# Kernel tuning notes

Hardware: AMD Instinct MI355X
Metric: run time of the kernel (lower is better)

The kernel has to match this reference:

```python
import jax, jax.numpy as jnp
import numpy as np

NUM_EMBEDDINGS = 8192
EMBEDDING_DIM = 256
COMMITMENT_COST = 0.25


def setup_inputs() -> dict:
    key = jax.random.key(0)
    k1, k2 = jax.random.split(key)
    z_e = jax.random.normal(k1, (16, 2048, EMBEDDING_DIM), dtype=jnp.float32)
    # nn.Embedding init: uniform(-1/K, 1/K)
    codebook = jax.random.uniform(
        k2, (NUM_EMBEDDINGS, EMBEDDING_DIM), dtype=jnp.float32,
        minval=-1.0 / NUM_EMBEDDINGS, maxval=1.0 / NUM_EMBEDDINGS)
    return {"z_e": z_e, "codebook": codebook}


def _nearest_indices(z_flat, codebook):
    # squared euclidean distances; argmin is identical to argmin of cdist
    # z_flat: [T, D], codebook: [K, D] -> dist2: [T, K]
    x2 = jnp.sum(z_flat * z_flat, axis=-1, keepdims=True)          # [T, 1]
    w2 = jnp.sum(codebook * codebook, axis=-1)                      # [K]
    xw = jnp.einsum('td,kd->tk', z_flat, codebook)                  # [T, K]
    dist2 = x2 - 2.0 * xw + w2
    return jnp.argmin(dist2, axis=1)                                # [T]


def reference(z_e, codebook):
    original_shape = z_e.shape
    z_e_flat = z_e.reshape(-1, EMBEDDING_DIM)
    indices = _nearest_indices(z_e_flat, codebook)
    z_q = codebook[indices].reshape(original_shape)
    # straight-through estimator
    z_q_ste = z_e + jax.lax.stop_gradient(z_q - z_e)
    commitment_loss = jnp.mean((z_e - jax.lax.stop_gradient(z_q_ste)) ** 2)
    codebook_loss = jnp.mean((z_q_ste - jax.lax.stop_gradient(z_e)) ** 2)
    loss = codebook_loss + COMMITMENT_COST * commitment_loss
    # codebook usage: fraction of unique indices (jit-friendly via scatter)
    used = jnp.zeros((NUM_EMBEDDINGS,), dtype=jnp.float32).at[indices].set(1.0)
    usage = jnp.sum(used) / NUM_EMBEDDINGS
    return (z_q_ste, loss, usage)
```

## Files before the change

### kernel.cpp

```cpp
#include <hip/hip_runtime.h>
#include <float.h>

#define T_TOTAL 32768
#define KC      8192
#define DIM     256

#define LOSS_IDX  ((size_t)T_TOTAL * DIM)
#define USAGE_IDX (LOSS_IDX + 1)

typedef short s16x8 __attribute__((ext_vector_type(8)));
typedef float f32x4 __attribute__((ext_vector_type(4)));

#define WS_W2    0
#define WS_FLAGS 32768
#define WS_CBF   65536

__device__ __forceinline__ unsigned short f2bf(float f) {
    unsigned int u = __float_as_uint(f);
    u += 0x7FFFu + ((u >> 16) & 1u);
    return (unsigned short)(u >> 16);
}

__global__ __launch_bounds__(256) void vq_prep(const float* __restrict__ cb,
                                               unsigned short* __restrict__ cbb,
                                               float* __restrict__ w2,
                                               int* __restrict__ flags,
                                               float* __restrict__ out) {
    const int blk = blockIdx.x, tid = threadIdx.x;
    size_t i = (size_t)blk * 2048 + (size_t)tid * 8;
    float4 a = *(const float4*)(cb + i);
    float4 b = *(const float4*)(cb + i + 4);
    uint4 o;
    o.x = (unsigned)f2bf(a.x) | ((unsigned)f2bf(a.y) << 16);
    o.y = (unsigned)f2bf(a.z) | ((unsigned)f2bf(a.w) << 16);
    o.z = (unsigned)f2bf(b.x) | ((unsigned)f2bf(b.y) << 16);
    o.w = (unsigned)f2bf(b.z) | ((unsigned)f2bf(b.w) << 16);
    *(uint4*)(cbb + i) = o;
    float s = a.x * a.x + a.y * a.y + a.z * a.z + a.w * a.w
            + b.x * b.x + b.y * b.y + b.z * b.z + b.w * b.w;
    #pragma unroll
    for (int m = 1; m <= 16; m <<= 1) s += __shfl_xor(s, m);
    if ((tid & 31) == 0) w2[blk * 8 + (tid >> 5)] = s;
    if (blk < 32) flags[blk * 256 + tid] = 0;
    if (blk == 0 && tid == 0) { out[LOSS_IDX] = 0.0f; out[USAGE_IDX] = 0.0f; }
}

__global__ __launch_bounds__(512, 2) void vq_main(const unsigned short* __restrict__ cbb,
                                                  const float* __restrict__ w2g,
                                                  const float* __restrict__ z_e,
                                                  const float* __restrict__ cb,
                                                  float* __restrict__ out,
                                                  int* __restrict__ flags) {
    __shared__ unsigned short ca[2][128 * 128];
    __shared__ unsigned long long smin[128];
    __shared__ float wls[8];

    const int tid  = threadIdx.x;
    const int lane = tid & 63;
    const int w    = tid >> 6;
    const int wr   = w >> 2;
    const int wc   = w & 3;
    const int quad = lane >> 4;
    const int l15  = lane & 15;
    const int t0   = blockIdx.x * 128;

    if (tid < 128) smin[tid] = ~0ULL;

    const int srow_off = lane >> 4;
    #define STAGE(CHUNK, KW, P)                                                         \
        {                                                                               \
            _Pragma("unroll")                                                           \
            for (int r = 0; r < 4; ++r) {                                               \
                int rowbase = r * 32 + w * 4;                                           \
                int row = rowbase + srow_off;                                           \
                int src_c = l15 ^ (row & 15);                                           \
                __builtin_amdgcn_global_load_lds(                                       \
                    (const __attribute__((address_space(1))) void*)                     \
                        (cbb + (size_t)((CHUNK) * 128 + row) * DIM + (KW) * 128 + src_c * 8), \
                    (__attribute__((address_space(3))) void*)(ca[P] + rowbase * 128),   \
                    16, 0, 0);                                                          \
            }                                                                           \
        }

    s16x8 af[4][8];
    #pragma unroll
    for (int i = 0; i < 4; ++i) {
        #pragma unroll
        for (int ks = 0; ks < 8; ++ks) {
            const float* p = z_e + (size_t)(t0 + wr * 64 + i * 16 + l15) * DIM + ks * 32 + quad * 8;
            float4 a = *(const float4*)p;
            float4 b = *(const float4*)(p + 4);
            s16x8 v;
            v[0] = (short)f2bf(a.x); v[1] = (short)f2bf(a.y);
            v[2] = (short)f2bf(a.z); v[3] = (short)f2bf(a.w);
            v[4] = (short)f2bf(b.x); v[5] = (short)f2bf(b.y);
            v[6] = (short)f2bf(b.z); v[7] = (short)f2bf(b.w);
            af[i][ks] = v;
        }
    }

    float best[4][4];
    int   bidx[4][4];
    #pragma unroll
    for (int i = 0; i < 4; ++i)
        #pragma unroll
        for (int r = 0; r < 4; ++r) { best[i][r] = FLT_MAX; bidx[i][r] = 0x7FFFFFFF; }

    STAGE(0, 0, 0);

    for (int c = 0; c < 64; ++c) {
        f32x4 acc[4][2];
        #pragma unroll
        for (int i = 0; i < 4; ++i)
            #pragma unroll
            for (int j = 0; j < 2; ++j) acc[i][j] = (f32x4){0.f, 0.f, 0.f, 0.f};

        #pragma unroll
        for (int kw = 0; kw < 2; ++kw) {
            __syncthreads();
            if (kw == 0) {
                STAGE(c, 1, 1);
            } else if (c < 63) {
                STAGE(c + 1, 0, 0);
            }
            #pragma unroll
            for (int kk = 0; kk < 4; ++kk) {
                s16x8 bfr[2];
                #pragma unroll
                for (int j = 0; j < 2; ++j) {
                    int row = wc * 32 + j * 16 + l15;
                    int slot = (kk * 4 + quad) ^ l15;
                    bfr[j] = *(const s16x8*)(ca[kw] + row * 128 + slot * 8);
                }
                #pragma unroll
                for (int i = 0; i < 4; ++i)
                    #pragma unroll
                    for (int j = 0; j < 2; ++j)
                        acc[i][j] = __builtin_amdgcn_mfma_f32_16x16x32_bf16(af[i][kw * 4 + kk], bfr[j], acc[i][j], 0, 0, 0);
            }
        }

        #pragma unroll
        for (int j = 0; j < 2; ++j) {
            int col = c * 128 + wc * 32 + j * 16 + l15;
            float w2v = w2g[col];
            #pragma unroll
            for (int i = 0; i < 4; ++i)
                #pragma unroll
                for (int r = 0; r < 4; ++r) {
                    float s = fmaf(-2.0f, acc[i][j][r], w2v);
                    if (s < best[i][r]) { best[i][r] = s; bidx[i][r] = col; }
                }
        }
    }

    #pragma unroll
    for (int i = 0; i < 4; ++i)
        #pragma unroll
        for (int r = 0; r < 4; ++r) {
            float b = best[i][r]; int ix = bidx[i][r];
            #pragma unroll
            for (int m = 1; m < 16; m <<= 1) {
                float ob = __shfl_xor(b, m);
                int   oi = __shfl_xor(ix, m);
                if (ob < b || (ob == b && oi < ix)) { b = ob; ix = oi; }
            }
            if (l15 == 0) {
                unsigned int fb = __float_as_uint(b);
                fb = (fb & 0x80000000u) ? ~fb : (fb | 0x80000000u);
                unsigned long long key = ((unsigned long long)fb << 32) | (unsigned int)ix;
                atomicMin(&smin[wr * 64 + i * 16 + quad * 4 + r], key);
            }
        }
    __syncthreads();

    float lsum = 0.0f;
    for (int t = w * 16; t < w * 16 + 16; ++t) {
        int tok = t0 + t;
        int k = (int)(unsigned int)(smin[t] & 0xFFFFFFFFull);
        if (lane == 0) flags[k] = 1;
        float4 cv = *(const float4*)(cb + (size_t)k * DIM + lane * 4);
        float4 zv = *(const float4*)(z_e + (size_t)tok * DIM + lane * 4);
        float dx = zv.x - cv.x, dy = zv.y - cv.y, dz = zv.z - cv.z, dw = zv.w - cv.w;
        lsum += dx * dx + dy * dy + dz * dz + dw * dw;
        *(float4*)(out + (size_t)tok * DIM + lane * 4) = cv;
    }
    #pragma unroll
    for (int m = 32; m >= 1; m >>= 1) lsum += __shfl_xor(lsum, m);
    if (lane == 0) wls[w] = lsum;
    __syncthreads();
    if (tid == 0) {
        float bsum = 0.0f;
        #pragma unroll
        for (int q = 0; q < 8; ++q) bsum += wls[q];
        atomicAdd(out + LOSS_IDX, bsum * (1.25f / (float)LOSS_IDX));
    }
}

__global__ __launch_bounds__(256) void vq_usage(const int* __restrict__ flags,
                                                float* __restrict__ out) {
    __shared__ int ws[4];
    int tid = threadIdx.x;
    int s = 0;
    for (int i = tid; i < KC; i += 256) s += flags[i];
    #pragma unroll
    for (int m = 32; m >= 1; m >>= 1) s += __shfl_xor(s, m);
    if ((tid & 63) == 0) ws[tid >> 6] = s;
    __syncthreads();
    if (tid == 0) out[USAGE_IDX] = (float)(ws[0] + ws[1] + ws[2] + ws[3]) / (float)KC;
}

extern "C" void kernel_launch(void* const* d_in, const int* in_sizes, int n_in,
                              void* d_out, int out_size, void* d_ws, size_t ws_size,
                              hipStream_t stream) {
    (void)in_sizes; (void)n_in; (void)out_size; (void)ws_size;
    const float* z_e = (const float*)d_in[0];
    const float* cb  = (const float*)d_in[1];
    float* out = (float*)d_out;

    char* ws = (char*)d_ws;
    float* w2    = (float*)(ws + WS_W2);
    int*   flags = (int*)(ws + WS_FLAGS);
    unsigned short* cbb = (unsigned short*)(ws + WS_CBF);

    vq_prep<<<KC / 8, 256, 0, stream>>>(cb, cbb, w2, flags, out);
    vq_main<<<T_TOTAL / 128, 512, 0, stream>>>(cbb, w2, z_e, cb, out, flags);
    vq_usage<<<1, 256, 0, stream>>>(flags, out);
}
```

Before: 265.5 us.

## Give each wave private double-buffered LDS tiles and drop block barriers

Each wave now stages only the 32 codebook rows it consumes into its own pair of LDS buffers. It waits on its own vector-memory counter instead of a block-wide __syncthreads, and the next window's load is issued after the current window's LDS fragments have been read. This is meant to remove barrier stalls between waves in the distance GEMM loop. In exchange, waves sharing a column group load the same codebook data twice. LDS use per block doubles to 128 KB, which likely prevents two blocks from fitting per CU.

```diff
diff --git a/kernel.cpp b/kernel.cpp
--- a/kernel.cpp
+++ b/kernel.cpp
@@ -51,7 +51,7 @@
                                                   const float* __restrict__ cb,
                                                   float* __restrict__ out,
                                                   int* __restrict__ flags) {
-    __shared__ unsigned short ca[2][128 * 128];
+    __shared__ unsigned short ca[16][4096];
     __shared__ unsigned long long smin[128];
     __shared__ float wls[8];
 
@@ -65,23 +65,26 @@
     const int t0   = blockIdx.x * 128;
 
     if (tid < 128) smin[tid] = ~0ULL;
-
-    const int srow_off = lane >> 4;
-    #define STAGE(CHUNK, KW, P)                                                         \
+    __syncthreads();
+
+    const int lrow_off = lane >> 4;
+    #define STAGE(WIN, P)                                                               \
         {                                                                               \
+            int _c  = (WIN) >> 1;                                                       \
+            int _kw = (WIN) & 1;                                                        \
             _Pragma("unroll")                                                           \
-            for (int r = 0; r < 4; ++r) {                                               \
-                int rowbase = r * 32 + w * 4;                                           \
-                int row = rowbase + srow_off;                                           \
-                int src_c = l15 ^ (row & 15);                                           \
+            for (int q = 0; q < 8; ++q) {                                               \
+                int lr = q * 4 + lrow_off;                                              \
+                int chunk = l15 ^ (lr & 15);                                            \
                 __builtin_amdgcn_global_load_lds(                                       \
                     (const __attribute__((address_space(1))) void*)                     \
-                        (cbb + (size_t)((CHUNK) * 128 + row) * DIM + (KW) * 128 + src_c * 8), \
-                    (__attribute__((address_space(3))) void*)(ca[P] + rowbase * 128),   \
+                        (cbb + (size_t)(_c * 128 + wc * 32 + lr) * DIM + _kw * 128 + chunk * 8), \
+                    (__attribute__((address_space(3))) void*)(&ca[w * 2 + (P)][q * 512]), \
                     16, 0, 0);                                                          \
             }                                                                           \
         }
 
+    STAGE(0, 0);
     s16x8 af[4][8];
     #pragma unroll
     for (int i = 0; i < 4; ++i) {
@@ -106,8 +109,6 @@
         #pragma unroll
         for (int r = 0; r < 4; ++r) { best[i][r] = FLT_MAX; bidx[i][r] = 0x7FFFFFFF; }
 
-    STAGE(0, 0, 0);
-
     for (int c = 0; c < 64; ++c) {
         f32x4 acc[4][2];
         #pragma unroll
@@ -117,27 +118,26 @@
 
         #pragma unroll
         for (int kw = 0; kw < 2; ++kw) {
-            __syncthreads();
-            if (kw == 0) {
-                STAGE(c, 1, 1);
-            } else if (c < 63) {
-                STAGE(c + 1, 0, 0);
-            }
-            #pragma unroll
-            for (int kk = 0; kk < 4; ++kk) {
-                s16x8 bfr[2];
+            const int win = c * 2 + kw;
+            const unsigned short* buf = ca[w * 2 + (win & 1)];
+            __builtin_amdgcn_s_waitcnt(0x0f70);
+            s16x8 bfr[4][2];
+            #pragma unroll
+            for (int kk = 0; kk < 4; ++kk)
                 #pragma unroll
                 for (int j = 0; j < 2; ++j) {
-                    int row = wc * 32 + j * 16 + l15;
+                    int row = j * 16 + l15;
                     int slot = (kk * 4 + quad) ^ l15;
-                    bfr[j] = *(const s16x8*)(ca[kw] + row * 128 + slot * 8);
+                    bfr[kk][j] = *(const s16x8*)(buf + row * 128 + slot * 8);
                 }
+            if (win < 127) STAGE(win + 1, (win + 1) & 1);
+            #pragma unroll
+            for (int kk = 0; kk < 4; ++kk)
                 #pragma unroll
                 for (int i = 0; i < 4; ++i)
                     #pragma unroll
                     for (int j = 0; j < 2; ++j)
-                        acc[i][j] = __builtin_amdgcn_mfma_f32_16x16x32_bf16(af[i][kw * 4 + kk], bfr[j], acc[i][j], 0, 0, 0);
-            }
+                        acc[i][j] = __builtin_amdgcn_mfma_f32_16x16x32_bf16(af[i][kw * 4 + kk], bfr[kk][j], acc[i][j], 0, 0, 0);
         }
 
         #pragma unroll
```

Result: faster. 253.7 us (-4.4%).
